# Performance work log

Hardware: AMD Instinct MI355X
Metric: run time of the kernel (lower is better)

## Reference

```python
import jax, jax.numpy as jnp
import numpy as np

EMBED = 128
HEADS = 4
HEAD_DIM = EMBED // HEADS

def setup_inputs() -> dict:
    key = jax.random.key(0)
    ks = jax.random.split(key, 8)
    N, S = 32, 1024
    values = jax.random.normal(ks[0], (N, S, EMBED), dtype=jnp.float32)
    keys_ = jax.random.normal(ks[1], (N, S, EMBED), dtype=jnp.float32)
    query = jax.random.normal(ks[2], (N, S, EMBED), dtype=jnp.float32)
    mask = jnp.ones((N, 1, S, S), dtype=jnp.int32)
    # nn.Linear weights: y = x @ W.T  (bias=False for q/k/v projections)
    sc = 1.0 / np.sqrt(HEAD_DIM)
    Wv = jax.random.uniform(ks[3], (HEAD_DIM, HEAD_DIM), jnp.float32, -sc, sc)
    Wk = jax.random.uniform(ks[4], (HEAD_DIM, HEAD_DIM), jnp.float32, -sc, sc)
    Wq = jax.random.uniform(ks[5], (HEAD_DIM, HEAD_DIM), jnp.float32, -sc, sc)
    so = 1.0 / np.sqrt(EMBED)
    Wo = jax.random.uniform(ks[6], (EMBED, EMBED), jnp.float32, -so, so)
    bo = jax.random.uniform(ks[7], (EMBED,), jnp.float32, -so, so)
    return {"values": values, "keys": keys_, "query": query, "mask": mask,
            "Wv": Wv, "Wk": Wk, "Wq": Wq, "Wo": Wo, "bo": bo}

def reference(values, keys, query, mask, Wv, Wk, Wq, Wo, bo):
    N = query.shape[0]
    # reshape to [N, S, H, D] and apply per-head linear projections (no bias)
    v = values.reshape(N, -1, HEADS, HEAD_DIM) @ Wv.T
    k = keys.reshape(N, -1, HEADS, HEAD_DIM) @ Wk.T
    q = query.reshape(N, -1, HEADS, HEAD_DIM) @ Wq.T
    # [N, H, Sq, Sk]
    att = jnp.einsum('nqhd,nkhd->nhqk', q, k)
    att = jnp.where(mask == 0, jnp.float32(-1e20), att)
    # NOTE: faithful to source: scale by sqrt(embed_size), not sqrt(head_dim)
    attention_weights = jax.nn.softmax(att / jnp.sqrt(jnp.float32(EMBED)), axis=3)
    out = jnp.einsum('nhql,nlhd->nqhd', attention_weights, v).reshape(N, -1, HEADS * HEAD_DIM)
    out = out @ Wo.T + bo
    return out, attention_weights
```

## Files before the change

### kernel.cpp

```cpp
#include <hip/hip_runtime.h>

#define SLEN 1024
#define NBATCH 32
#define NHEADS 4
#define HDIM 32
#define EMB 128
#define LSTRIDE 1032

typedef short short8 __attribute__((ext_vector_type(8)));
typedef short short4v __attribute__((ext_vector_type(4)));
typedef float floatx4 __attribute__((ext_vector_type(4)));
typedef int   intx4  __attribute__((ext_vector_type(4)));

__device__ __forceinline__ unsigned short f2bf(float f) {
    unsigned u = __float_as_uint(f);
    u += 0x7fffu + ((u >> 16) & 1u);
    return (unsigned short)(u >> 16);
}
__device__ __forceinline__ float bf2f(unsigned short h) {
    return __uint_as_float(((unsigned)h) << 16);
}

__global__ __launch_bounds__(256) void proj_kernel(
    const float* __restrict__ vals, const float* __restrict__ keys,
    const float* __restrict__ qrys,
    const float* __restrict__ Wv, const float* __restrict__ Wk,
    const float* __restrict__ Wq, const float* __restrict__ Wo,
    unsigned short* __restrict__ qb, unsigned short* __restrict__ kb,
    unsigned short* __restrict__ vt, unsigned short* __restrict__ wo_bf)
{
    int b = blockIdx.x;
    int tid = threadIdx.x;
    if (b == 512) {
        #pragma unroll
        for (int i = 0; i < 64; ++i) {
            int idx = tid + (i << 8);
            wo_bf[idx] = f2bf(Wo[idx]);
        }
        return;
    }
    int n = b >> 4;
    int s0 = (b & 15) << 6;
    int wave = tid >> 6, lane = tid & 63;
    int quad = lane >> 4, l16 = lane & 15;
    int srow = s0 + (wave << 4);

    short8 bw[3][2];
    const float* Ws[3] = { Wv, Wk, Wq };
    const float scal[3] = { 1.0f, 1.0f, 0.08838834764831845f };
    #pragma unroll
    for (int t = 0; t < 3; ++t) {
        float s = scal[t];
        #pragma unroll
        for (int hh = 0; hh < 2; ++hh) {
            const float* wp = Ws[t] + (hh * 16 + l16) * 32 + quad * 8;
            float4 w0 = *(const float4*)wp;
            float4 w1 = *(const float4*)(wp + 4);
            short8 r;
            r[0] = (short)f2bf(w0.x * s); r[1] = (short)f2bf(w0.y * s);
            r[2] = (short)f2bf(w0.z * s); r[3] = (short)f2bf(w0.w * s);
            r[4] = (short)f2bf(w1.x * s); r[5] = (short)f2bf(w1.y * s);
            r[6] = (short)f2bf(w1.z * s); r[7] = (short)f2bf(w1.w * s);
            bw[t][hh] = r;
        }
    }

    const float* srcs[3] = { vals, keys, qrys };
    #pragma unroll
    for (int t = 0; t < 3; ++t) {
        const float* src = srcs[t];
        #pragma unroll
        for (int h = 0; h < NHEADS; ++h) {
            size_t nh = (size_t)(n * NHEADS + h);
            const float* xp = src + ((size_t)(n * SLEN + srow + l16) * EMB + h * HDIM + quad * 8);
            float4 x0 = *(const float4*)xp;
            float4 x1 = *(const float4*)(xp + 4);
            short8 a;
            a[0] = (short)f2bf(x0.x); a[1] = (short)f2bf(x0.y);
            a[2] = (short)f2bf(x0.z); a[3] = (short)f2bf(x0.w);
            a[4] = (short)f2bf(x1.x); a[5] = (short)f2bf(x1.y);
            a[6] = (short)f2bf(x1.z); a[7] = (short)f2bf(x1.w);
            floatx4 c0 = {0.f, 0.f, 0.f, 0.f};
            floatx4 c1 = {0.f, 0.f, 0.f, 0.f};
            c0 = __builtin_amdgcn_mfma_f32_16x16x32_bf16(a, bw[t][0], c0, 0, 0, 0);
            c1 = __builtin_amdgcn_mfma_f32_16x16x32_bf16(a, bw[t][1], c1, 0, 0, 0);
            if (t == 0) {
                short4v p0, p1;
                p0[0] = (short)f2bf(c0[0]); p0[1] = (short)f2bf(c0[1]);
                p0[2] = (short)f2bf(c0[2]); p0[3] = (short)f2bf(c0[3]);
                p1[0] = (short)f2bf(c1[0]); p1[1] = (short)f2bf(c1[1]);
                p1[2] = (short)f2bf(c1[2]); p1[3] = (short)f2bf(c1[3]);
                *(short4v*)(vt + (nh * HDIM + l16) * SLEN + srow + quad * 4) = p0;
                *(short4v*)(vt + (nh * HDIM + 16 + l16) * SLEN + srow + quad * 4) = p1;
            } else {
                unsigned short* dst = (t == 1 ? kb : qb) +
                    (nh * SLEN + srow + quad * 4) * HDIM;
                #pragma unroll
                for (int r = 0; r < 4; ++r) {
                    dst[r * HDIM + l16]      = f2bf(c0[r]);
                    dst[r * HDIM + 16 + l16] = f2bf(c1[r]);
                }
            }
        }
    }
}

__global__ __launch_bounds__(256, 3) void attn_kernel(
    const unsigned short* __restrict__ qb, const unsigned short* __restrict__ kb,
    const unsigned short* __restrict__ vt, const int* __restrict__ mask,
    float* __restrict__ wout, unsigned short* __restrict__ attnv)
{
    __shared__ unsigned short eb[16 * LSTRIDE];
    __shared__ unsigned long long mb[16][17];
    __shared__ float partial[4][16][32];
    __shared__ __align__(16) float redmax[16][4];
    __shared__ __align__(16) float redsum[16][4];

    int bid = blockIdx.x;
    int n = bid >> 6;
    int r0 = (bid & 63) << 4;
    int tid = threadIdx.x;
    int wave = tid >> 6, lane = tid & 63;
    int quad = lane >> 4, l16 = lane & 15;
    int srow = tid >> 4, c16 = tid & 15;

    {
        unsigned long long mbits = 0ull;
        const int* mrow = mask + (size_t)(n * SLEN + r0 + srow) * SLEN;
        #pragma unroll
        for (int i = 0; i < 8; ++i) {
            int cb = (c16 + (i << 4)) << 3;
            intx4 a  = __builtin_nontemporal_load((const intx4*)(mrow + cb));
            intx4 bq = __builtin_nontemporal_load((const intx4*)(mrow + cb + 4));
            unsigned bits = 0;
            bits |= (unsigned)(a[0] != 0);
            bits |= (unsigned)(a[1] != 0) << 1;
            bits |= (unsigned)(a[2] != 0) << 2;
            bits |= (unsigned)(a[3] != 0) << 3;
            bits |= (unsigned)(bq[0] != 0) << 4;
            bits |= (unsigned)(bq[1] != 0) << 5;
            bits |= (unsigned)(bq[2] != 0) << 6;
            bits |= (unsigned)(bq[3] != 0) << 7;
            mbits |= (unsigned long long)bits << (i * 8);
        }
        mb[srow][c16] = mbits;
    }
    __syncthreads();

    unsigned long long lmask = 0ull;
    {
        int qh = quad >> 1, ql = quad & 1;
        int shbase = (wave << 4) + (ql << 2);
        #pragma unroll
        for (int t = 0; t < 16; ++t) {
            unsigned long long ch = mb[l16][((t << 1) + qh) & 15];
            unsigned long long nib = (ch >> (shbase + ((t >> 3) << 3))) & 0xFull;
            lmask |= nib << (t << 2);
        }
    }

    for (int h = 0; h < NHEADS; ++h) {
        size_t nh = (size_t)(n * NHEADS + h);

        short8 qfrag = *(const short8*)(qb + (nh * SLEN + r0 + l16) * HDIM + quad * 8);
        const unsigned short* kbase = kb + (nh * SLEN + (wave << 8)) * HDIM;

        floatx4 c[16];
        float mx = -3.0e38f;
        #pragma unroll
        for (int t = 0; t < 16; ++t) {
            short8 kfrag = *(const short8*)(kbase + (size_t)((t << 4) + l16) * HDIM + quad * 8);
            floatx4 acc = {0.f, 0.f, 0.f, 0.f};
            acc = __builtin_amdgcn_mfma_f32_16x16x32_bf16(kfrag, qfrag, acc, 0, 0, 0);
            unsigned nb = (unsigned)(lmask >> (t << 2)) & 15u;
            #pragma unroll
            for (int r = 0; r < 4; ++r) {
                float x = ((nb >> r) & 1u) ? acc[r] : -1e20f;
                acc[r] = x;
                mx = fmaxf(mx, x);
            }
            c[t] = acc;
        }
        mx = fmaxf(mx, __shfl_xor(mx, 16));
        mx = fmaxf(mx, __shfl_xor(mx, 32));
        if (quad == 0) redmax[l16][wave] = mx;
        __syncthreads();
        {
            floatx4 mv = *(const floatx4*)&redmax[l16][0];
            mx = fmaxf(fmaxf(mv[0], mv[1]), fmaxf(mv[2], mv[3]));
        }

        float sum = 0.f;
        unsigned short* erow = eb + l16 * LSTRIDE + (wave << 8);
        #pragma unroll
        for (int t = 0; t < 16; ++t) {
            floatx4 cc = c[t];
            float e0 = __expf(cc[0] - mx);
            float e1 = __expf(cc[1] - mx);
            float e2 = __expf(cc[2] - mx);
            float e3 = __expf(cc[3] - mx);
            sum += (e0 + e1) + (e2 + e3);
            cc[0] = e0; cc[1] = e1; cc[2] = e2; cc[3] = e3;
            c[t] = cc;
            short4v p;
            p[0] = (short)f2bf(e0); p[1] = (short)f2bf(e1);
            p[2] = (short)f2bf(e2); p[3] = (short)f2bf(e3);
            *(short4v*)(erow + (t << 4) + (quad << 2)) = p;
        }
        sum += __shfl_xor(sum, 16);
        sum += __shfl_xor(sum, 32);
        if (quad == 0) redsum[l16][wave] = sum;
        __syncthreads();
        float inv;
        {
            floatx4 sv = *(const floatx4*)&redsum[l16][0];
            inv = 1.0f / ((sv[0] + sv[1]) + (sv[2] + sv[3]));
        }

        float* wrow = wout + (nh * SLEN + r0 + l16) * SLEN + (wave << 8);
        #pragma unroll
        for (int t = 0; t < 16; ++t) {
            floatx4 wv;
            wv[0] = c[t][0] * inv; wv[1] = c[t][1] * inv;
            wv[2] = c[t][2] * inv; wv[3] = c[t][3] * inv;
            __builtin_nontemporal_store(wv, (floatx4*)(wrow + (t << 4) + (quad << 2)));
        }

        floatx4 acc0 = {0.f, 0.f, 0.f, 0.f}, acc1 = {0.f, 0.f, 0.f, 0.f};
        const unsigned short* vbase = vt + nh * HDIM * SLEN;
        #pragma unroll
        for (int i = 0; i < 8; ++i) {
            int kt = (wave << 3) + i;
            short8 a8 = *(const short8*)(eb + l16 * LSTRIDE + (kt << 5) + (quad << 3));
            short8 b0 = *(const short8*)(vbase + (size_t)l16 * SLEN + (kt << 5) + (quad << 3));
            short8 b1 = *(const short8*)(vbase + (size_t)(16 + l16) * SLEN + (kt << 5) + (quad << 3));
            acc0 = __builtin_amdgcn_mfma_f32_16x16x32_bf16(a8, b0, acc0, 0, 0, 0);
            acc1 = __builtin_amdgcn_mfma_f32_16x16x32_bf16(a8, b1, acc1, 0, 0, 0);
        }
        #pragma unroll
        for (int r = 0; r < 4; ++r) {
            partial[wave][quad * 4 + r][l16] = acc0[r];
            partial[wave][quad * 4 + r][16 + l16] = acc1[r];
        }
        __syncthreads();

        {
            int m = srow;
            int d0 = c16 << 1;
            float s0 = partial[0][m][d0] + partial[1][m][d0] +
                       partial[2][m][d0] + partial[3][m][d0];
            float s1 = partial[0][m][d0 + 1] + partial[1][m][d0 + 1] +
                       partial[2][m][d0 + 1] + partial[3][m][d0 + 1];
            floatx4 sv = *(const floatx4*)&redsum[m][0];
            float iv = 1.0f / ((sv[0] + sv[1]) + (sv[2] + sv[3]));
            unsigned pk = (unsigned)f2bf(s0 * iv) | ((unsigned)f2bf(s1 * iv) << 16);
            __builtin_nontemporal_store(pk,
                (unsigned*)(attnv + (size_t)(n * SLEN + r0 + m) * EMB + h * HDIM + d0));
        }
    }
}

__global__ __launch_bounds__(256) void out_kernel(
    const unsigned short* __restrict__ attnv, const unsigned short* __restrict__ wo_bf,
    const float* __restrict__ bo, float* __restrict__ out)
{
    int tid = threadIdx.x;
    int wave = tid >> 6, lane = tid & 63;
    int quad = lane >> 4, l16 = lane & 15;
    int m0 = blockIdx.x * 64 + (wave << 4);

    short8 afr[4];
    const unsigned short* ap = attnv + (size_t)(m0 + l16) * EMB + quad * 8;
    #pragma unroll
    for (int ks = 0; ks < 4; ++ks) afr[ks] = *(const short8*)(ap + ks * 32);

    #pragma unroll
    for (int ct = 0; ct < 8; ++ct) {
        floatx4 c = {0.f, 0.f, 0.f, 0.f};
        const unsigned short* bp = wo_bf + ((ct << 4) + l16) * EMB + quad * 8;
        #pragma unroll
        for (int ks = 0; ks < 4; ++ks) {
            short8 b = *(const short8*)(bp + ks * 32);
            c = __builtin_amdgcn_mfma_f32_16x16x32_bf16(afr[ks], b, c, 0, 0, 0);
        }
        int col = (ct << 4) + l16;
        float bias = bo[col];
        #pragma unroll
        for (int r = 0; r < 4; ++r)
            __builtin_nontemporal_store(c[r] + bias,
                &out[(size_t)(m0 + quad * 4 + r) * EMB + col]);
    }
}

extern "C" void kernel_launch(void* const* d_in, const int* in_sizes, int n_in,
                              void* d_out, int out_size, void* d_ws, size_t ws_size,
                              hipStream_t stream)
{
    (void)in_sizes; (void)n_in; (void)out_size; (void)ws_size;
    const float* vals = (const float*)d_in[0];
    const float* keys = (const float*)d_in[1];
    const float* qrys = (const float*)d_in[2];
    const int*   mask = (const int*)d_in[3];
    const float* Wv   = (const float*)d_in[4];
    const float* Wk   = (const float*)d_in[5];
    const float* Wq   = (const float*)d_in[6];
    const float* Wo   = (const float*)d_in[7];
    const float* bo   = (const float*)d_in[8];
    float* out = (float*)d_out;

    const size_t NHS = (size_t)NBATCH * NHEADS * SLEN * HDIM;
    unsigned short* ws = (unsigned short*)d_ws;
    unsigned short* qb    = ws;
    unsigned short* kbuf  = qb + NHS;
    unsigned short* vt    = kbuf + NHS;
    unsigned short* av    = vt + NHS;
    unsigned short* wo_bf = av + (size_t)NBATCH * SLEN * EMB;
    float* wout = out + (size_t)NBATCH * SLEN * EMB;

    hipLaunchKernelGGL(proj_kernel, dim3(513), dim3(256), 0, stream,
                       vals, keys, qrys, Wv, Wk, Wq, Wo, qb, kbuf, vt, wo_bf);
    hipLaunchKernelGGL(attn_kernel, dim3(NBATCH * 64), dim3(256), 0, stream,
                       qb, kbuf, vt, mask, wout, av);
    hipLaunchKernelGGL(out_kernel, dim3((NBATCH * SLEN) / 64), dim3(256), 0, stream,
                       av, wo_bf, bo, out);
}
```

Baseline: 786.0 us.

## Fuse output projection into attention kernel and drop per-head max barrier

Each wave now uses its local row max for the exponentials. After one barrier it combines per-wave max and sum statistics, flash-style, to rescale both the stored weights and the PV partials, removing one __syncthreads per head. The output projection kernel is folded into the attention kernel: the per-block attention outputs are kept in shared memory and multiplied by Wo at the end. This removes the global attnv round trip and one launch, at the cost of extra shared memory that may reduce occupancy, and extra exp work.

```diff
diff --git a/kernel.cpp b/kernel.cpp
--- a/kernel.cpp
+++ b/kernel.cpp
@@ -6,6 +6,7 @@
 #define HDIM 32
 #define EMB 128
 #define LSTRIDE 1032
+#define AVS 136
 
 typedef short short8 __attribute__((ext_vector_type(8)));
 typedef short short4v __attribute__((ext_vector_type(4)));
@@ -108,13 +109,16 @@
 __global__ __launch_bounds__(256, 3) void attn_kernel(
     const unsigned short* __restrict__ qb, const unsigned short* __restrict__ kb,
     const unsigned short* __restrict__ vt, const int* __restrict__ mask,
-    float* __restrict__ wout, unsigned short* __restrict__ attnv)
+    const unsigned short* __restrict__ wo_bf, const float* __restrict__ bo,
+    float* __restrict__ wout, float* __restrict__ out)
 {
     __shared__ unsigned short eb[16 * LSTRIDE];
     __shared__ unsigned long long mb[16][17];
     __shared__ float partial[4][16][32];
-    __shared__ __align__(16) float redmax[16][4];
-    __shared__ __align__(16) float redsum[16][4];
+    __shared__ __align__(16) float redmax[2][16][4];
+    __shared__ __align__(16) float redsum[2][16][4];
+    __shared__ __align__(16) float scl[2][16][4];
+    __shared__ unsigned short avls[16][AVS];
 
     int bid = blockIdx.x;
     int n = bid >> 6;
@@ -161,6 +165,7 @@
 
     for (int h = 0; h < NHEADS; ++h) {
         size_t nh = (size_t)(n * NHEADS + h);
+        int p = h & 1;
 
         short8 qfrag = *(const short8*)(qb + (nh * SLEN + r0 + l16) * HDIM + quad * 8);
         const unsigned short* kbase = kb + (nh * SLEN + (wave << 8)) * HDIM;
@@ -183,12 +188,6 @@
         }
         mx = fmaxf(mx, __shfl_xor(mx, 16));
         mx = fmaxf(mx, __shfl_xor(mx, 32));
-        if (quad == 0) redmax[l16][wave] = mx;
-        __syncthreads();
-        {
-            floatx4 mv = *(const floatx4*)&redmax[l16][0];
-            mx = fmaxf(fmaxf(mv[0], mv[1]), fmaxf(mv[2], mv[3]));
-        }
 
         float sum = 0.f;
         unsigned short* erow = eb + l16 * LSTRIDE + (wave << 8);
@@ -202,27 +201,40 @@
             sum += (e0 + e1) + (e2 + e3);
             cc[0] = e0; cc[1] = e1; cc[2] = e2; cc[3] = e3;
             c[t] = cc;
-            short4v p;
-            p[0] = (short)f2bf(e0); p[1] = (short)f2bf(e1);
-            p[2] = (short)f2bf(e2); p[3] = (short)f2bf(e3);
-            *(short4v*)(erow + (t << 4) + (quad << 2)) = p;
+            short4v pk;
+            pk[0] = (short)f2bf(e0); pk[1] = (short)f2bf(e1);
+            pk[2] = (short)f2bf(e2); pk[3] = (short)f2bf(e3);
+            *(short4v*)(erow + (t << 4) + (quad << 2)) = pk;
         }
         sum += __shfl_xor(sum, 16);
         sum += __shfl_xor(sum, 32);
-        if (quad == 0) redsum[l16][wave] = sum;
+        if (quad == 0) {
+            redmax[p][l16][wave] = mx;
+            redsum[p][l16][wave] = sum;
+        }
         __syncthreads();
-        float inv;
+
+        float factor, inv;
         {
-            floatx4 sv = *(const floatx4*)&redsum[l16][0];
-            inv = 1.0f / ((sv[0] + sv[1]) + (sv[2] + sv[3]));
+            floatx4 mv = *(const floatx4*)&redmax[p][l16][0];
+            floatx4 sv = *(const floatx4*)&redsum[p][l16][0];
+            float M = fmaxf(fmaxf(mv[0], mv[1]), fmaxf(mv[2], mv[3]));
+            float t0 = sv[0] * __expf(mv[0] - M);
+            float t1 = sv[1] * __expf(mv[1] - M);
+            float t2 = sv[2] * __expf(mv[2] - M);
+            float t3 = sv[3] * __expf(mv[3] - M);
+            inv = 1.0f / ((t0 + t1) + (t2 + t3));
+            float myscale = __expf(mx - M);
+            factor = inv * myscale;
+            if (quad == 0) scl[p][l16][wave] = factor;
         }
 
         float* wrow = wout + (nh * SLEN + r0 + l16) * SLEN + (wave << 8);
         #pragma unroll
         for (int t = 0; t < 16; ++t) {
             floatx4 wv;
-            wv[0] = c[t][0] * inv; wv[1] = c[t][1] * inv;
-            wv[2] = c[t][2] * inv; wv[3] = c[t][3] * inv;
+            wv[0] = c[t][0] * factor; wv[1] = c[t][1] * factor;
+            wv[2] = c[t][2] * factor; wv[3] = c[t][3] * factor;
             __builtin_nontemporal_store(wv, (floatx4*)(wrow + (t << 4) + (quad << 2)));
         }
 
@@ -247,48 +259,40 @@
         {
             int m = srow;
             int d0 = c16 << 1;
-            float s0 = partial[0][m][d0] + partial[1][m][d0] +
-                       partial[2][m][d0] + partial[3][m][d0];
-            float s1 = partial[0][m][d0 + 1] + partial[1][m][d0 + 1] +
-                       partial[2][m][d0 + 1] + partial[3][m][d0 + 1];
-            floatx4 sv = *(const floatx4*)&redsum[m][0];
-            float iv = 1.0f / ((sv[0] + sv[1]) + (sv[2] + sv[3]));
-            unsigned pk = (unsigned)f2bf(s0 * iv) | ((unsigned)f2bf(s1 * iv) << 16);
-            __builtin_nontemporal_store(pk,
-                (unsigned*)(attnv + (size_t)(n * SLEN + r0 + m) * EMB + h * HDIM + d0));
-        }
-    }
-}
-
-__global__ __launch_bounds__(256) void out_kernel(
-    const unsigned short* __restrict__ attnv, const unsigned short* __restrict__ wo_bf,
-    const float* __restrict__ bo, float* __restrict__ out)
-{
-    int tid = threadIdx.x;
-    int wave = tid >> 6, lane = tid & 63;
-    int quad = lane >> 4, l16 = lane & 15;
-    int m0 = blockIdx.x * 64 + (wave << 4);
-
-    short8 afr[4];
-    const unsigned short* ap = attnv + (size_t)(m0 + l16) * EMB + quad * 8;
-    #pragma unroll
-    for (int ks = 0; ks < 4; ++ks) afr[ks] = *(const short8*)(ap + ks * 32);
-
-    #pragma unroll
-    for (int ct = 0; ct < 8; ++ct) {
-        floatx4 c = {0.f, 0.f, 0.f, 0.f};
-        const unsigned short* bp = wo_bf + ((ct << 4) + l16) * EMB + quad * 8;
-        #pragma unroll
-        for (int ks = 0; ks < 4; ++ks) {
-            short8 b = *(const short8*)(bp + ks * 32);
-            c = __builtin_amdgcn_mfma_f32_16x16x32_bf16(afr[ks], b, c, 0, 0, 0);
-        }
-        int col = (ct << 4) + l16;
-        float bias = bo[col];
-        #pragma unroll
-        for (int r = 0; r < 4; ++r)
-            __builtin_nontemporal_store(c[r] + bias,
-                &out[(size_t)(m0 + quad * 4 + r) * EMB + col]);
+            floatx4 sc = *(const floatx4*)&scl[p][m][0];
+            float s0 = partial[0][m][d0] * sc[0] + partial[1][m][d0] * sc[1] +
+                       partial[2][m][d0] * sc[2] + partial[3][m][d0] * sc[3];
+            float s1 = partial[0][m][d0 + 1] * sc[0] + partial[1][m][d0 + 1] * sc[1] +
+                       partial[2][m][d0 + 1] * sc[2] + partial[3][m][d0 + 1] * sc[3];
+            unsigned pk = (unsigned)f2bf(s0) | ((unsigned)f2bf(s1) << 16);
+            *(unsigned*)&avls[m][h * HDIM + d0] = pk;
+        }
+    }
+    __syncthreads();
+
+    {
+        short8 afr[4];
+        const unsigned short* ap = &avls[l16][quad * 8];
+        #pragma unroll
+        for (int ks = 0; ks < 4; ++ks) afr[ks] = *(const short8*)(ap + ks * 32);
+
+        #pragma unroll
+        for (int cc = 0; cc < 2; ++cc) {
+            int ct = (wave << 1) + cc;
+            floatx4 acc = {0.f, 0.f, 0.f, 0.f};
+            const unsigned short* bp = wo_bf + ((ct << 4) + l16) * EMB + quad * 8;
+            #pragma unroll
+            for (int ks = 0; ks < 4; ++ks) {
+                short8 b8 = *(const short8*)(bp + ks * 32);
+                acc = __builtin_amdgcn_mfma_f32_16x16x32_bf16(afr[ks], b8, acc, 0, 0, 0);
+            }
+            int col = (ct << 4) + l16;
+            float bias = bo[col];
+            #pragma unroll
+            for (int r = 0; r < 4; ++r)
+                __builtin_nontemporal_store(acc[r] + bias,
+                    &out[(size_t)(n * SLEN + r0 + quad * 4 + r) * EMB + col]);
+        }
     }
 }
 
@@ -313,14 +317,11 @@
     unsigned short* qb    = ws;
     unsigned short* kbuf  = qb + NHS;
     unsigned short* vt    = kbuf + NHS;
-    unsigned short* av    = vt + NHS;
-    unsigned short* wo_bf = av + (size_t)NBATCH * SLEN * EMB;
+    unsigned short* wo_bf = vt + NHS;
     float* wout = out + (size_t)NBATCH * SLEN * EMB;
 
     hipLaunchKernelGGL(proj_kernel, dim3(513), dim3(256), 0, stream,
                        vals, keys, qrys, Wv, Wk, Wq, Wo, qb, kbuf, vt, wo_bf);
     hipLaunchKernelGGL(attn_kernel, dim3(NBATCH * 64), dim3(256), 0, stream,
-                       qb, kbuf, vt, mask, wout, av);
-    hipLaunchKernelGGL(out_kernel, dim3((NBATCH * SLEN) / 64), dim3(256), 0, stream,
-                       av, wo_bf, bo, out);
-}
+                       qb, kbuf, vt, mask, wo_bf, bo, wout, out);
+}
```

After: 773.0 us. Within noise of the previous version (-1.7%).
